# Optimization experiments

Measured on AMD Instinct MI355X. Metric: run time of the kernel, lower is better.

The kernel has to match this reference:

```python
import jax, jax.numpy as jnp
import numpy as np

B, N, D = 2, 2048, 1024
H, DH = 16, 64
DI = 4096
EPS = 1e-5
NEG_SLOPE = 0.01  # F.leaky_relu default


def _ln(x, g, b):
    mu = jnp.mean(x, axis=-1, keepdims=True)
    var = jnp.mean((x - mu) ** 2, axis=-1, keepdims=True)
    return (x - mu) * jax.lax.rsqrt(var + EPS) * g + b


def setup_inputs() -> dict:
    key = jax.random.key(0)
    ks = jax.random.split(key, 10)
    s = 0.02
    return {
        "Z": jax.random.normal(ks[0], (B, N, D), jnp.float32),
        "new_mask": jax.random.normal(ks[1], (B, N, N), jnp.float32),
        "mask": jax.random.uniform(ks[2], (B, N, N), jnp.float32),
        "ln1_g": jnp.ones((D,), jnp.float32),
        "ln1_b": jnp.zeros((D,), jnp.float32),
        "qkv_w": jax.random.normal(ks[3], (3 * D, D), jnp.float32) * s,
        "qkv_b": jnp.zeros((3 * D,), jnp.float32),
        "o_w": jax.random.normal(ks[4], (D, H * DH), jnp.float32) * s,
        "ln2_g": jnp.ones((D,), jnp.float32),
        "ln2_b": jnp.zeros((D,), jnp.float32),
        "p1_w": jax.random.normal(ks[5], (DI, D), jnp.float32) * s,
        "p1_b": jnp.zeros((DI,), jnp.float32),
        "p2_w": jax.random.normal(ks[6], (D, DI), jnp.float32) * s,
        "p2_b": jnp.zeros((D,), jnp.float32),
    }


def reference(Z, new_mask, mask, ln1_g, ln1_b, qkv_w, qkv_b, o_w, ln2_g, ln2_b, p1_w, p1_b, p2_w, p2_b):
    inp = Z
    Zn = _ln(Z, ln1_g, ln1_b)
    qkv = (Zn @ qkv_w.T + qkv_b).reshape(B, N, H, 3 * DH)
    # torch chunk order in the source: V, Q, K
    V, Q, K = jnp.split(qkv, 3, axis=3)  # each [B,N,H,DH]
    # scores: einsum('bnij,bmij->binm') == [B,H,N,N]
    W = jnp.einsum("bnhd,bmhd->bhnm", Q, K) / np.sqrt(DH) + new_mask[:, None]
    A = jax.nn.softmax(W, axis=3) * mask[:, None]
    attn = jnp.einsum("bhnm,bmhd->bnhd", A, V).reshape(B, N, D)
    attn = jnp.where(attn >= 0, attn, NEG_SLOPE * attn) @ o_w.T  # leaky_relu then o_net (no bias)
    Z1 = attn + inp
    Zn2 = _ln(Z1, ln2_g, ln2_b)
    h = jax.nn.relu(Zn2 @ p1_w.T + p1_b)
    return h @ p2_w.T + p2_b + Z1
```

## Files before the change

kernel.cpp:

```cpp
#include <hip/hip_runtime.h>

typedef unsigned short u16;
typedef __attribute__((ext_vector_type(8))) short bf16x8;
typedef __attribute__((ext_vector_type(4))) float f32x4;

#define DEV static __device__ __forceinline__

DEV u16 f2bf(float f) {
    unsigned u = __float_as_uint(f);
    u += 0x7FFFu + ((u >> 16) & 1u);
    return (u16)(u >> 16);
}

typedef const __attribute__((address_space(1))) void* gas1_t;
typedef __attribute__((address_space(3))) void* gas3_t;

DEV void gl_lds16(const u16* g, u16* l) {
    __builtin_amdgcn_global_load_lds((gas1_t)g, (gas3_t)l, 16, 0, 0);
}

DEV int sw8(int row, int chunk) { return row * 64 + ((chunk ^ (row & 7)) << 3); }

__global__ __launch_bounds__(256) void prep_all(const float* __restrict__ qkv_w,
                                                const float* __restrict__ o_w,
                                                const float* __restrict__ p1_w,
                                                const float* __restrict__ p2_w,
                                                const float* __restrict__ qkv_b,
                                                const float* __restrict__ nm,
                                                const float* __restrict__ pm,
                                                u16* __restrict__ qkvW,
                                                u16* __restrict__ oW,
                                                u16* __restrict__ p1W,
                                                u16* __restrict__ p2W,
                                                float* __restrict__ pbias,
                                                unsigned* __restrict__ Mp) {
    const int bid = blockIdx.x, t = threadIdx.x;
    if (bid < 3072) {
        int i = bid * 256 + t;
        int orow = i >> 8, cc = i & 255;
        int region = orow >> 10, rem = orow & 1023, h = rem >> 6, tt = rem & 63;
        int srow = h * 192 + region * 64 + tt;
        float4 v = ((const float4*)qkv_w)[srow * 256 + cc];
        ushort4 o;
        o.x = f2bf(v.x); o.y = f2bf(v.y); o.z = f2bf(v.z); o.w = f2bf(v.w);
        ((ushort4*)qkvW)[i] = o;
    } else if (bid < 4096) {
        int i = (bid - 3072) * 256 + t;
        float4 v = ((const float4*)o_w)[i];
        ushort4 o;
        o.x = f2bf(v.x); o.y = f2bf(v.y); o.z = f2bf(v.z); o.w = f2bf(v.w);
        ((ushort4*)oW)[i] = o;
    } else if (bid < 8192) {
        int i = (bid - 4096) * 256 + t;
        float4 v = ((const float4*)p1_w)[i];
        ushort4 o;
        o.x = f2bf(v.x); o.y = f2bf(v.y); o.z = f2bf(v.z); o.w = f2bf(v.w);
        ((ushort4*)p1W)[i] = o;
    } else if (bid < 12288) {
        int i = (bid - 8192) * 256 + t;
        float4 v = ((const float4*)p2_w)[i];
        ushort4 o;
        o.x = f2bf(v.x); o.y = f2bf(v.y); o.z = f2bf(v.z); o.w = f2bf(v.w);
        ((ushort4*)p2W)[i] = o;
    } else if (bid < 20480) {
        int i = (bid - 12288) * 256 + t;
        float4 a = ((const float4*)nm)[i];
        float4 b = ((const float4*)pm)[i];
        uint4 o;
        o.x = ((unsigned)f2bf(b.x) << 16) | f2bf(a.x * 1.4426950f);
        o.y = ((unsigned)f2bf(b.y) << 16) | f2bf(a.y * 1.4426950f);
        o.z = ((unsigned)f2bf(b.z) << 16) | f2bf(a.z * 1.4426950f);
        o.w = ((unsigned)f2bf(b.w) << 16) | f2bf(a.w * 1.4426950f);
        ((uint4*)Mp)[i] = o;
    } else {
#pragma unroll
        for (int k = 0; k < 12; k++) {
            int i = k * 256 + t;
            int region = i >> 10, rem = i & 1023, h = rem >> 6, tt = rem & 63;
            pbias[i] = qkv_b[h * 192 + region * 64 + tt];
        }
    }
}

__global__ __launch_bounds__(256) void ln_bf16(const float* __restrict__ x,
                                               const float* __restrict__ gam,
                                               const float* __restrict__ bet,
                                               u16* __restrict__ y) {
    const int row = blockIdx.x;
    const int t = threadIdx.x;
    const float4 v = ((const float4*)(x + (size_t)row * 1024))[t];
    float s = v.x + v.y + v.z + v.w;
    float ss = v.x * v.x + v.y * v.y + v.z * v.z + v.w * v.w;
#pragma unroll
    for (int o = 1; o < 64; o <<= 1) {
        s += __shfl_xor(s, o);
        ss += __shfl_xor(ss, o);
    }
    __shared__ float rs[4], rss[4];
    const int wave = t >> 6, lane = t & 63;
    if (lane == 0) { rs[wave] = s; rss[wave] = ss; }
    __syncthreads();
    const float tot = rs[0] + rs[1] + rs[2] + rs[3];
    const float totss = rss[0] + rss[1] + rss[2] + rss[3];
    const float mu = tot * (1.0f / 1024.0f);
    const float var = totss * (1.0f / 1024.0f) - mu * mu;
    const float rstd = rsqrtf(var + 1e-5f);
    const float4 g4 = ((const float4*)gam)[t];
    const float4 b4 = ((const float4*)bet)[t];
    ushort4 o;
    o.x = f2bf((v.x - mu) * rstd * g4.x + b4.x);
    o.y = f2bf((v.y - mu) * rstd * g4.y + b4.y);
    o.z = f2bf((v.z - mu) * rstd * g4.z + b4.z);
    o.w = f2bf((v.w - mu) * rstd * g4.w + b4.w);
    ((ushort4*)(y + (size_t)row * 1024))[t] = o;
}

__global__ __launch_bounds__(256) void ln2_comb4(const float* __restrict__ p0,
                                                 const float* __restrict__ p1,
                                                 const float* __restrict__ p2,
                                                 const float* __restrict__ p3,
                                                 const float* __restrict__ Z,
                                                 const float* __restrict__ gam,
                                                 const float* __restrict__ bet,
                                                 float* __restrict__ Z1,
                                                 u16* __restrict__ y) {
    const int row = blockIdx.x;
    const int t = threadIdx.x;
    const size_t off = (size_t)row * 256 + t;
    const float4 a = ((const float4*)p0)[off];
    const float4 c = ((const float4*)p1)[off];
    const float4 d = ((const float4*)p2)[off];
    const float4 e = ((const float4*)p3)[off];
    const float4 z = ((const float4*)Z)[off];
    float4 v;
    v.x = a.x + c.x + d.x + e.x + z.x;
    v.y = a.y + c.y + d.y + e.y + z.y;
    v.z = a.z + c.z + d.z + e.z + z.z;
    v.w = a.w + c.w + d.w + e.w + z.w;
    ((float4*)Z1)[off] = v;
    float s = v.x + v.y + v.z + v.w;
    float ss = v.x * v.x + v.y * v.y + v.z * v.z + v.w * v.w;
#pragma unroll
    for (int o = 1; o < 64; o <<= 1) {
        s += __shfl_xor(s, o);
        ss += __shfl_xor(ss, o);
    }
    __shared__ float rs[4], rss[4];
    const int wave = t >> 6, lane = t & 63;
    if (lane == 0) { rs[wave] = s; rss[wave] = ss; }
    __syncthreads();
    const float tot = rs[0] + rs[1] + rs[2] + rs[3];
    const float totss = rss[0] + rss[1] + rss[2] + rss[3];
    const float mu = tot * (1.0f / 1024.0f);
    const float var = totss * (1.0f / 1024.0f) - mu * mu;
    const float rstd = rsqrtf(var + 1e-5f);
    const float4 g4 = ((const float4*)gam)[t];
    const float4 b4 = ((const float4*)bet)[t];
    ushort4 o;
    o.x = f2bf((v.x - mu) * rstd * g4.x + b4.x);
    o.y = f2bf((v.y - mu) * rstd * g4.y + b4.y);
    o.z = f2bf((v.z - mu) * rstd * g4.z + b4.z);
    o.w = f2bf((v.w - mu) * rstd * g4.w + b4.w);
    ((ushort4*)(y + (size_t)row * 1024))[t] = o;
}

__global__ __launch_bounds__(256) void out_comb(const float* __restrict__ p0,
                                                const float* __restrict__ p1,
                                                const float* __restrict__ bias,
                                                const float* __restrict__ Z1,
                                                float* __restrict__ out) {
    int i = blockIdx.x * 256 + threadIdx.x;
    float4 a = ((const float4*)p0)[i];
    float4 c = ((const float4*)p1)[i];
    float4 z = ((const float4*)Z1)[i];
    float4 b = ((const float4*)bias)[i & 255];
    float4 o;
    o.x = a.x + c.x + z.x + b.x; o.y = a.y + c.y + z.y + b.y;
    o.z = a.z + c.z + z.z + b.z; o.w = a.w + c.w + z.w + b.w;
    ((float4*)out)[i] = o;
}

template <int EPI>
__global__ __launch_bounds__(256, 3) void gemm_bt(const u16* __restrict__ A,
                                                  const u16* __restrict__ Bt,
                                                  const float* __restrict__ bias,
                                                  void* __restrict__ out0,
                                                  void* __restrict__ out1,
                                                  void* __restrict__ out2,
                                                  int M, int N, int K, int ldk) {
    __shared__ __align__(16) u16 As[128 * 32];
    __shared__ __align__(16) u16 Bs[128 * 32];
    const int tid = threadIdx.x;
    const int wave = tid >> 6, lane = tid & 63;
    const int lhi = lane >> 4, llo = lane & 15;
    const int bx = blockIdx.x, by = blockIdx.y;
    const int kz = blockIdx.z * K;

    const int arow = wave * 32 + (lane >> 2);
    const int acol = (lane & 3) * 8;
    const u16* gA = A + (size_t)(by * 128 + arow) * ldk + kz + acol;
    const u16* gB = Bt + (size_t)(bx * 128 + arow) * ldk + kz + acol;
    u16* lA = As + wave * 1024 + lane * 8;
    u16* lB = Bs + wave * 1024 + lane * 8;

    const int wr = wave >> 1, wc = wave & 1;
    const f32x4 zero = {0.f, 0.f, 0.f, 0.f};
    f32x4 acc[4][4];
#pragma unroll
    for (int i = 0; i < 4; i++)
#pragma unroll
        for (int j = 0; j < 4; j++) acc[i][j] = zero;

    for (int k0 = 0; k0 < K; k0 += 32) {
        __syncthreads();
        gl_lds16(gA, lA);
        gl_lds16(gA + 16 * (size_t)ldk, lA + 512);
        gl_lds16(gB, lB);
        gl_lds16(gB + 16 * (size_t)ldk, lB + 512);
        gA += 32; gB += 32;
        __syncthreads();
        bf16x8 af[4], bfr[4];
#pragma unroll
        for (int i = 0; i < 4; i++)
            af[i] = *(const bf16x8*)(As + (wr * 64 + i * 16 + llo) * 32 + lhi * 8);
#pragma unroll
        for (int j = 0; j < 4; j++)
            bfr[j] = *(const bf16x8*)(Bs + (wc * 64 + j * 16 + llo) * 32 + lhi * 8);
#pragma unroll
        for (int i = 0; i < 4; i++)
#pragma unroll
            for (int j = 0; j < 4; j++)
                acc[i][j] = __builtin_amdgcn_mfma_f32_16x16x32_bf16(af[i], bfr[j], acc[i][j], 0, 0, 0);
    }

    const int rbase = by * 128 + wr * 64 + lhi * 4;
    const int cbase = bx * 128 + wc * 64 + llo;
    float* pout = nullptr;
    if constexpr (EPI == 4) {
        pout = (blockIdx.z < 2) ? ((float*)out0 + (size_t)blockIdx.z * M * N)
                                : ((float*)out1 + (size_t)(blockIdx.z - 2) * M * N);
    }
#pragma unroll
    for (int i = 0; i < 4; i++) {
#pragma unroll
        for (int j = 0; j < 4; j++) {
#pragma unroll
            for (int r = 0; r < 4; r++) {
                const int row = rbase + i * 16 + r;
                const int col = cbase + j * 16;
                float v = acc[i][j][r];
                if constexpr (EPI == 0) {
                    v += bias[col];
                    const int region = col >> 10;
                    const int c = col & 1023;
                    const int b = row >> 11, n = row & 2047;
                    if (region == 0) {
                        ((float*)out0)[(size_t)row * 1024 + c] = v;
                    } else {
                        const int h = c >> 6, t = c & 63;
                        u16* dst = (region == 1) ? (u16*)out1 : (u16*)out2;
                        dst[(((size_t)(b * 16 + h)) * 2048 + n) * 64 + t] = f2bf(v);
                    }
                } else if constexpr (EPI == 2) {
                    v += bias[col];
                    v = v > 0.f ? v : 0.f;
                    ((u16*)out0)[(size_t)row * N + col] = f2bf(v);
                } else {
                    pout[(size_t)row * N + col] = v;
                }
            }
        }
    }
}

__global__ __launch_bounds__(256) void vtrans(const float* __restrict__ Vsc,
                                              u16* __restrict__ Vt) {
    __shared__ u16 Ts[64 * 72];
    const int nt = blockIdx.x;
    const int bh = blockIdx.y;
    const int b = bh >> 4, h = bh & 15;
    const int t = threadIdx.x;
    const int n0 = nt * 64;
    const int nr = t >> 2;
    const int dq = (t & 3) * 16;
    const float* src = Vsc + ((size_t)(b * 2048 + n0 + nr)) * 1024 + h * 64 + dq;
    float4 v0 = ((const float4*)src)[0];
    float4 v1 = ((const float4*)src)[1];
    float4 v2 = ((const float4*)src)[2];
    float4 v3 = ((const float4*)src)[3];
    u16* c0 = Ts + nr;
    c0[(dq + 0) * 72]  = f2bf(v0.x); c0[(dq + 1) * 72]  = f2bf(v0.y);
    c0[(dq + 2) * 72]  = f2bf(v0.z); c0[(dq + 3) * 72]  = f2bf(v0.w);
    c0[(dq + 4) * 72]  = f2bf(v1.x); c0[(dq + 5) * 72]  = f2bf(v1.y);
    c0[(dq + 6) * 72]  = f2bf(v1.z); c0[(dq + 7) * 72]  = f2bf(v1.w);
    c0[(dq + 8) * 72]  = f2bf(v2.x); c0[(dq + 9) * 72]  = f2bf(v2.y);
    c0[(dq + 10) * 72] = f2bf(v2.z); c0[(dq + 11) * 72] = f2bf(v2.w);
    c0[(dq + 12) * 72] = f2bf(v3.x); c0[(dq + 13) * 72] = f2bf(v3.y);
    c0[(dq + 14) * 72] = f2bf(v3.z); c0[(dq + 15) * 72] = f2bf(v3.w);
    __syncthreads();
    const int d = t >> 2, n8 = (t & 3) * 16;
    bf16x8 o0 = *(const bf16x8*)(Ts + d * 72 + n8);
    bf16x8 o1 = *(const bf16x8*)(Ts + d * 72 + n8 + 8);
    u16* dst = Vt + ((size_t)bh * 64 + d) * 2048 + n0 + n8;
    *(bf16x8*)dst = o0;
    *(bf16x8*)(dst + 8) = o1;
}

__global__ __launch_bounds__(256, 4) void attn_fused4(const u16* __restrict__ Qg,
                                                      const u16* __restrict__ Kg,
                                                      const u16* __restrict__ Vt,
                                                      const unsigned* __restrict__ Mp,
                                                      u16* __restrict__ attnL) {
    __shared__ __align__(16) u16 Qs[64 * 64];
    __shared__ __align__(16) u16 Ks[64 * 64];
    __shared__ __align__(16) u16 Vs[64 * 64];
    __shared__ __align__(16) u16 Ps[64 * 72];
    const int tid = threadIdx.x, wave = tid >> 6, lane = tid & 63;
    const int lhi = lane >> 4, llo = lane & 15;
    const int id = blockIdx.x;
    const int hh = id >> 6, rem = id & 63;
    const int b = rem >> 5, qt = rem & 31;
    const int bh = b * 16 + hh;
    const int q0 = qt * 64;
    const int l3 = lane >> 3, l7 = lane & 7;
    const int swcol = (l7 ^ (l3 & 7)) * 8;

#pragma unroll
    for (int s = 0; s < 2; s++) {
        const int row = wave * 16 + s * 8 + l3;
        gl_lds16(Qg + ((size_t)bh * 2048 + q0 + row) * 64 + swcol,
                 Qs + wave * 1024 + s * 512 + lane * 8);
    }

    const unsigned* Mpb = Mp + (size_t)b * 2048 * 2048;
    int midx[4];
#pragma unroll
    for (int r = 0; r < 4; r++)
        midx[r] = (q0 + wave * 16 + lhi * 4 + r) * 2048 + llo;

    const f32x4 zero = {0.f, 0.f, 0.f, 0.f};
    f32x4 accO[4];
    float lsum[4];
#pragma unroll
    for (int j = 0; j < 4; j++) accO[j] = zero;
#pragma unroll
    for (int r = 0; r < 4; r++) lsum[r] = 0.f;

    const float CS = 0.125f * 1.4426950f;
    const int pb0 = (wave * 16 + lhi * 4) * 72 + llo;

    for (int m0 = 0; m0 < 2048; m0 += 64) {
        __syncthreads();
#pragma unroll
        for (int s = 0; s < 2; s++) {
            const int row = wave * 16 + s * 8 + l3;
            gl_lds16(Kg + ((size_t)bh * 2048 + m0 + row) * 64 + swcol,
                     Ks + wave * 1024 + s * 512 + lane * 8);
            gl_lds16(Vt + ((size_t)bh * 64 + row) * 2048 + m0 + swcol,
                     Vs + wave * 1024 + s * 512 + lane * 8);
        }
        unsigned mv[4][4];
#pragma unroll
        for (int r = 0; r < 4; r++)
#pragma unroll
            for (int j = 0; j < 4; j++) mv[r][j] = Mpb[midx[r] + m0 + j * 16];
        __syncthreads();

        f32x4 sacc[4];
#pragma unroll
        for (int j = 0; j < 4; j++) sacc[j] = zero;
#pragma unroll
        for (int kk = 0; kk < 2; kk++) {
            const bf16x8 aq = *(const bf16x8*)(Qs + sw8(wave * 16 + llo, kk * 4 + lhi));
#pragma unroll
            for (int j = 0; j < 4; j++) {
                const bf16x8 bk = *(const bf16x8*)(Ks + sw8(j * 16 + llo, kk * 4 + lhi));
                sacc[j] = __builtin_amdgcn_mfma_f32_16x16x32_bf16(aq, bk, sacc[j], 0, 0, 0);
            }
        }

#pragma unroll
        for (int j = 0; j < 4; j++)
#pragma unroll
            for (int r = 0; r < 4; r++) {
                const unsigned u = mv[r][j];
                const float nm = __uint_as_float(u << 16);
                const float pm = __uint_as_float(u & 0xFFFF0000u);
                const float e = exp2f(fmaf(sacc[j][r], CS, nm));
                lsum[r] += e;
                const float p = e * pm;
                Ps[pb0 + r * 72 + j * 16] = (u16)(__float_as_uint(p) >> 16);
            }

#pragma unroll
        for (int kk = 0; kk < 2; kk++) {
            const bf16x8 ap = *(const bf16x8*)(Ps + (wave * 16 + llo) * 72 + kk * 32 + lhi * 8);
#pragma unroll
            for (int jd = 0; jd < 4; jd++) {
                const bf16x8 bv = *(const bf16x8*)(Vs + sw8(jd * 16 + llo, kk * 4 + lhi));
                accO[jd] = __builtin_amdgcn_mfma_f32_16x16x32_bf16(ap, bv, accO[jd], 0, 0, 0);
            }
        }
    }

#pragma unroll
    for (int r = 0; r < 4; r++) {
#pragma unroll
        for (int o = 1; o < 16; o <<= 1) lsum[r] += __shfl_xor(lsum[r], o);
        lsum[r] = 1.0f / lsum[r];
    }
#pragma unroll
    for (int jd = 0; jd < 4; jd++)
#pragma unroll
        for (int r = 0; r < 4; r++) {
            float v = accO[jd][r] * lsum[r];
            v = v >= 0.f ? v : 0.01f * v;
            const int q = q0 + wave * 16 + lhi * 4 + r;
            attnL[((size_t)b * 2048 + q) * 1024 + hh * 64 + jd * 16 + llo] = f2bf(v);
        }
}

extern "C" void kernel_launch(void* const* d_in, const int* in_sizes, int n_in,
                              void* d_out, int out_size, void* d_ws, size_t ws_size,
                              hipStream_t stream) {
    const float* Z     = (const float*)d_in[0];
    const float* nmask = (const float*)d_in[1];
    const float* pmask = (const float*)d_in[2];
    const float* ln1_g = (const float*)d_in[3];
    const float* ln1_b = (const float*)d_in[4];
    const float* qkv_w = (const float*)d_in[5];
    const float* qkv_b = (const float*)d_in[6];
    const float* o_w   = (const float*)d_in[7];
    const float* ln2_g = (const float*)d_in[8];
    const float* ln2_b = (const float*)d_in[9];
    const float* p1_w  = (const float*)d_in[10];
    const float* p1_b  = (const float*)d_in[11];
    const float* p2_w  = (const float*)d_in[12];
    const float* p2_b  = (const float*)d_in[13];
    float* out = (float*)d_out;

    char* w = (char*)d_ws;
    auto take = [&](size_t bytes) -> char* {
        char* p = w;
        w += (bytes + 255) & ~(size_t)255;
        return p;
    };
    u16* qkvW   = (u16*)take((size_t)3072 * 1024 * 2);
    u16* oW     = (u16*)take((size_t)1024 * 1024 * 2);
    u16* p1W    = (u16*)take((size_t)4096 * 1024 * 2);
    u16* p2W    = (u16*)take((size_t)1024 * 4096 * 2);
    u16* Zn     = (u16*)take((size_t)4096 * 1024 * 2);
    u16* Qb     = (u16*)take((size_t)32 * 2048 * 64 * 2);
    u16* Kb     = (u16*)take((size_t)32 * 2048 * 64 * 2);
    u16* Vt     = (u16*)take((size_t)32 * 64 * 2048 * 2);
    u16* attnL  = (u16*)take((size_t)4096 * 1024 * 2);
    float* Z1   = (float*)take((size_t)4096 * 1024 * 4);
    u16* hbuf   = (u16*)take((size_t)4096 * 4096 * 2);
    unsigned* Mp = (unsigned*)take((size_t)2 * 2048 * 2048 * 4);
    float* pbias = (float*)take((size_t)3072 * 4);
    float* Vsc    = (float*)hbuf;
    float* part01 = (float*)Mp;
    float* part23 = (float*)hbuf;

    prep_all<<<dim3(20481), 256, 0, stream>>>(qkv_w, o_w, p1_w, p2_w, qkv_b, nmask, pmask,
                                              qkvW, oW, p1W, p2W, pbias, Mp);
    ln_bf16<<<dim3(4096), 256, 0, stream>>>(Z, ln1_g, ln1_b, Zn);
    gemm_bt<0><<<dim3(24, 32), 256, 0, stream>>>(Zn, qkvW, pbias, Vsc, Qb, Kb, 4096, 3072, 1024, 1024);
    vtrans<<<dim3(32, 32), 256, 0, stream>>>(Vsc, Vt);
    attn_fused4<<<dim3(1024), 256, 0, stream>>>(Qb, Kb, Vt, Mp, attnL);
    gemm_bt<4><<<dim3(8, 32, 4), 256, 0, stream>>>(attnL, oW, nullptr, part01, part23, nullptr,
                                                   4096, 1024, 256, 1024);
    ln2_comb4<<<dim3(4096), 256, 0, stream>>>(part01, part01 + (size_t)4096 * 1024,
                                              part23, part23 + (size_t)4096 * 1024,
                                              Z, ln2_g, ln2_b, Z1, Zn);
    gemm_bt<2><<<dim3(32, 32), 256, 0, stream>>>(Zn, p1W, p1_b, hbuf, nullptr, nullptr,
                                                 4096, 4096, 1024, 1024);
    gemm_bt<4><<<dim3(8, 32, 2), 256, 0, stream>>>(hbuf, p2W, nullptr, part01, nullptr, nullptr,
                                                   4096, 1024, 2048, 4096);
    out_comb<<<dim3(4096), 256, 0, stream>>>(part01, part01 + (size_t)4096 * 1024, p2_b, Z1, out);
}
```

Before: 442.2 us.

## Rewrite attention with 32x32 MFMA, register P, double-buffered K/V, tiled mask layout

Result: slower. 458.8 us (+3.7%).

```diff
diff --git a/kernel.cpp b/kernel.cpp
--- a/kernel.cpp
+++ b/kernel.cpp
@@ -3,6 +3,8 @@
 typedef unsigned short u16;
 typedef __attribute__((ext_vector_type(8))) short bf16x8;
 typedef __attribute__((ext_vector_type(4))) float f32x4;
+typedef __attribute__((ext_vector_type(16))) float f32x16;
+typedef __attribute__((ext_vector_type(4))) unsigned u32x4;
 
 #define DEV static __device__ __forceinline__
 
@@ -17,6 +19,12 @@
 
 DEV void gl_lds16(const u16* g, u16* l) {
     __builtin_amdgcn_global_load_lds((gas1_t)g, (gas3_t)l, 16, 0, 0);
+}
+
+DEV unsigned cvtpk_bf16(float a, float b) {
+    unsigned r;
+    asm("v_cvt_pk_bf16_f32 %0, %1, %2" : "=v"(r) : "v"(a), "v"(b));
+    return r;
 }
 
 DEV int sw8(int row, int chunk) { return row * 64 + ((chunk ^ (row & 7)) << 3); }
@@ -71,7 +79,17 @@
         o.y = ((unsigned)f2bf(b.y) << 16) | f2bf(a.y * 1.4426950f);
         o.z = ((unsigned)f2bf(b.z) << 16) | f2bf(a.z * 1.4426950f);
         o.w = ((unsigned)f2bf(b.w) << 16) | f2bf(a.w * 1.4426950f);
-        ((uint4*)Mp)[i] = o;
+        int e = i * 4;
+        int bb = e >> 22;
+        int rem = e & 4194303;
+        int n = rem >> 11;
+        int m = rem & 2047;
+        int mt = m >> 5;
+        int j = m & 31;
+        int hi = (j >> 2) & 1;
+        int rb4 = j >> 3;
+        size_t oi = (((size_t)(bb * 64 + mt) * 2048 + n) * 2 + hi) * 4 + rb4;
+        ((uint4*)Mp)[oi] = o;
     } else {
 #pragma unroll
         for (int k = 0; k < 12; k++) {
@@ -306,118 +324,151 @@
     *(bf16x8*)(dst + 8) = o1;
 }
 
-__global__ __launch_bounds__(256, 4) void attn_fused4(const u16* __restrict__ Qg,
+DEV void stage_kv(const u16* __restrict__ Kg, const u16* __restrict__ Vtg,
+                  u16* ks, u16* vs, int bh, int m0, int wave, int lane) {
+    const int l3 = lane >> 3, l7 = lane & 7;
+    const int swcol = (l7 ^ l3) << 3;
+#pragma unroll
+    for (int s = 0; s < 2; s++) {
+        const int row = wave * 16 + s * 8 + l3;
+        gl_lds16(Kg + ((size_t)bh * 2048 + m0 + row) * 64 + swcol,
+                 ks + wave * 1024 + s * 512 + lane * 8);
+        gl_lds16(Vtg + ((size_t)bh * 64 + row) * 2048 + m0 + swcol,
+                 vs + wave * 1024 + s * 512 + lane * 8);
+    }
+}
+
+__global__ __launch_bounds__(256, 4) void attn_fused5(const u16* __restrict__ Qg,
                                                       const u16* __restrict__ Kg,
-                                                      const u16* __restrict__ Vt,
+                                                      const u16* __restrict__ Vtg,
                                                       const unsigned* __restrict__ Mp,
                                                       u16* __restrict__ attnL) {
-    __shared__ __align__(16) u16 Qs[64 * 64];
-    __shared__ __align__(16) u16 Ks[64 * 64];
-    __shared__ __align__(16) u16 Vs[64 * 64];
-    __shared__ __align__(16) u16 Ps[64 * 72];
+    __shared__ __align__(16) u16 Ks[2][64 * 64];
+    __shared__ __align__(16) u16 Vs[2][64 * 64];
+    __shared__ float lsh[2][32], lsh2[2][32];
     const int tid = threadIdx.x, wave = tid >> 6, lane = tid & 63;
-    const int lhi = lane >> 4, llo = lane & 15;
+    const int qh = wave & 1, wm = wave >> 1;
+    const int hi = lane >> 5, l31 = lane & 31;
     const int id = blockIdx.x;
     const int hh = id >> 6, rem = id & 63;
     const int b = rem >> 5, qt = rem & 31;
     const int bh = b * 16 + hh;
     const int q0 = qt * 64;
-    const int l3 = lane >> 3, l7 = lane & 7;
-    const int swcol = (l7 ^ (l3 & 7)) * 8;
-
-#pragma unroll
-    for (int s = 0; s < 2; s++) {
-        const int row = wave * 16 + s * 8 + l3;
-        gl_lds16(Qg + ((size_t)bh * 2048 + q0 + row) * 64 + swcol,
-                 Qs + wave * 1024 + s * 512 + lane * 8);
-    }
-
-    const unsigned* Mpb = Mp + (size_t)b * 2048 * 2048;
-    int midx[4];
-#pragma unroll
-    for (int r = 0; r < 4; r++)
-        midx[r] = (q0 + wave * 16 + lhi * 4 + r) * 2048 + llo;
-
-    const f32x4 zero = {0.f, 0.f, 0.f, 0.f};
-    f32x4 accO[4];
-    float lsum[4];
-#pragma unroll
-    for (int j = 0; j < 4; j++) accO[j] = zero;
-#pragma unroll
-    for (int r = 0; r < 4; r++) lsum[r] = 0.f;
-
+
+    stage_kv(Kg, Vtg, Ks[0], Vs[0], bh, 0, wave, lane);
+    const int qrow = q0 + qh * 32 + l31;
+    const u16* qptr = Qg + ((size_t)bh * 2048 + qrow) * 64 + hi * 8;
+    bf16x8 qf[4];
+#pragma unroll
+    for (int ks = 0; ks < 4; ks++) qf[ks] = *(const bf16x8*)(qptr + ks * 16);
+
+    const unsigned* mptr = Mp + (size_t)b * 4194304 + (size_t)wm * 65536
+                              + (size_t)qrow * 32 + hi * 16;
+
+    const f32x16 z16 = {0.f,0.f,0.f,0.f,0.f,0.f,0.f,0.f,0.f,0.f,0.f,0.f,0.f,0.f,0.f,0.f};
+    f32x16 accO[2];
+    accO[0] = z16; accO[1] = z16;
+    float lsum = 0.f;
     const float CS = 0.125f * 1.4426950f;
-    const int pb0 = (wave * 16 + lhi * 4) * 72 + llo;
-
-    for (int m0 = 0; m0 < 2048; m0 += 64) {
+    const bool h1 = (hi != 0);
+    __syncthreads();
+
+    for (int t = 0; t < 32; t++) {
+        const int cur = t & 1;
+        const uint4* mp4 = (const uint4*)(mptr + (size_t)t * 131072);
+        const uint4 mva = mp4[0], mvb = mp4[1], mvc = mp4[2], mvd = mp4[3];
+        if (t < 31) stage_kv(Kg, Vtg, Ks[cur ^ 1], Vs[cur ^ 1], bh, (t + 1) * 64, wave, lane);
+
+        const u16* ksb = Ks[cur];
+        f32x16 sacc = z16;
+        __builtin_amdgcn_s_setprio(1);
+#pragma unroll
+        for (int ks = 0; ks < 4; ks++) {
+            const bf16x8 kf = *(const bf16x8*)(ksb + sw8(wm * 32 + l31, ks * 2 + hi));
+            sacc = __builtin_amdgcn_mfma_f32_32x32x16_bf16(kf, qf[ks], sacc, 0, 0, 0);
+        }
+        __builtin_amdgcn_s_setprio(0);
+
+        const unsigned mm[16] = {mva.x, mva.y, mva.z, mva.w, mvb.x, mvb.y, mvb.z, mvb.w,
+                                 mvc.x, mvc.y, mvc.z, mvc.w, mvd.x, mvd.y, mvd.z, mvd.w};
+        float p[16];
+#pragma unroll
+        for (int r = 0; r < 16; r++) {
+            const unsigned u = mm[r];
+            const float e = exp2f(fmaf(sacc[r], CS, __uint_as_float(u << 16)));
+            lsum += e;
+            p[r] = e * __uint_as_float(u & 0xFFFF0000u);
+        }
+        const unsigned w0 = cvtpk_bf16(p[0], p[1]),   w1 = cvtpk_bf16(p[2], p[3]);
+        const unsigned w2 = cvtpk_bf16(p[4], p[5]),   w3 = cvtpk_bf16(p[6], p[7]);
+        const unsigned w4 = cvtpk_bf16(p[8], p[9]),   w5 = cvtpk_bf16(p[10], p[11]);
+        const unsigned w6 = cvtpk_bf16(p[12], p[13]), w7 = cvtpk_bf16(p[14], p[15]);
+        const unsigned o0 = (unsigned)__shfl_xor((int)w0, 32);
+        const unsigned o1 = (unsigned)__shfl_xor((int)w1, 32);
+        const unsigned o2 = (unsigned)__shfl_xor((int)w2, 32);
+        const unsigned o3 = (unsigned)__shfl_xor((int)w3, 32);
+        const unsigned o4 = (unsigned)__shfl_xor((int)w4, 32);
+        const unsigned o5 = (unsigned)__shfl_xor((int)w5, 32);
+        const unsigned o6 = (unsigned)__shfl_xor((int)w6, 32);
+        const unsigned o7 = (unsigned)__shfl_xor((int)w7, 32);
+        const u32x4 fa0 = {h1 ? o2 : w0, h1 ? o3 : w1, h1 ? w2 : o0, h1 ? w3 : o1};
+        const u32x4 fa1 = {h1 ? o6 : w4, h1 ? o7 : w5, h1 ? w6 : o4, h1 ? w7 : o5};
+        const bf16x8 pa0 = __builtin_bit_cast(bf16x8, fa0);
+        const bf16x8 pa1 = __builtin_bit_cast(bf16x8, fa1);
+
+        const u16* vsb = Vs[cur];
+        __builtin_amdgcn_s_setprio(1);
+#pragma unroll
+        for (int dh = 0; dh < 2; dh++) {
+            const bf16x8 vf0 = *(const bf16x8*)(vsb + sw8(dh * 32 + l31, wm * 4 + hi));
+            accO[dh] = __builtin_amdgcn_mfma_f32_32x32x16_bf16(pa0, vf0, accO[dh], 0, 0, 0);
+            const bf16x8 vf1 = *(const bf16x8*)(vsb + sw8(dh * 32 + l31, wm * 4 + 2 + hi));
+            accO[dh] = __builtin_amdgcn_mfma_f32_32x32x16_bf16(pa1, vf1, accO[dh], 0, 0, 0);
+        }
+        __builtin_amdgcn_s_setprio(0);
         __syncthreads();
-#pragma unroll
-        for (int s = 0; s < 2; s++) {
-            const int row = wave * 16 + s * 8 + l3;
-            gl_lds16(Kg + ((size_t)bh * 2048 + m0 + row) * 64 + swcol,
-                     Ks + wave * 1024 + s * 512 + lane * 8);
-            gl_lds16(Vt + ((size_t)bh * 64 + row) * 2048 + m0 + swcol,
-                     Vs + wave * 1024 + s * 512 + lane * 8);
-        }
-        unsigned mv[4][4];
-#pragma unroll
-        for (int r = 0; r < 4; r++)
-#pragma unroll
-            for (int j = 0; j < 4; j++) mv[r][j] = Mpb[midx[r] + m0 + j * 16];
-        __syncthreads();
-
-        f32x4 sacc[4];
-#pragma unroll
-        for (int j = 0; j < 4; j++) sacc[j] = zero;
-#pragma unroll
-        for (int kk = 0; kk < 2; kk++) {
-            const bf16x8 aq = *(const bf16x8*)(Qs + sw8(wave * 16 + llo, kk * 4 + lhi));
-#pragma unroll
-            for (int j = 0; j < 4; j++) {
-                const bf16x8 bk = *(const bf16x8*)(Ks + sw8(j * 16 + llo, kk * 4 + lhi));
-                sacc[j] = __builtin_amdgcn_mfma_f32_16x16x32_bf16(aq, bk, sacc[j], 0, 0, 0);
+    }
+
+    const float lsum2 = lsum + __shfl_xor(lsum, 32);
+    float* cb = (float*)&Ks[0][0];
+    if (wm == 1) {
+        float* dst = cb + (size_t)(qh * 64 + lane) * 32;
+#pragma unroll
+        for (int dh = 0; dh < 2; dh++)
+#pragma unroll
+            for (int c = 0; c < 4; c++) {
+                const f32x4 v = {accO[dh][c * 4 + 0], accO[dh][c * 4 + 1],
+                                 accO[dh][c * 4 + 2], accO[dh][c * 4 + 3]};
+                *(f32x4*)(dst + dh * 16 + c * 4) = v;
+            }
+        if (lane < 32) lsh[qh][lane] = lsum2;
+    }
+    __syncthreads();
+    if (wm == 0) {
+        const float* src = cb + (size_t)(qh * 64 + lane) * 32;
+        const float lt = lsum2 + lsh[qh][l31];
+#pragma unroll
+        for (int dh = 0; dh < 2; dh++)
+#pragma unroll
+            for (int c = 0; c < 16; c++)
+                accO[dh][c] += src[dh * 16 + c];
+        if (lane < 32) lsh2[qh][lane] = 1.0f / lt;
+    }
+    __syncthreads();
+    if (wm == 0) {
+#pragma unroll
+        for (int r = 0; r < 16; r++) {
+            const int ql = (r & 3) + 8 * (r >> 2) + 4 * hi;
+            const float linv = lsh2[qh][ql];
+            const int qg = q0 + qh * 32 + ql;
+#pragma unroll
+            for (int dh = 0; dh < 2; dh++) {
+                float v = accO[dh][r] * linv;
+                v = v >= 0.f ? v : 0.01f * v;
+                attnL[((size_t)b * 2048 + qg) * 1024 + hh * 64 + dh * 32 + l31] = f2bf(v);
             }
         }
-
-#pragma unroll
-        for (int j = 0; j < 4; j++)
-#pragma unroll
-            for (int r = 0; r < 4; r++) {
-                const unsigned u = mv[r][j];
-                const float nm = __uint_as_float(u << 16);
-                const float pm = __uint_as_float(u & 0xFFFF0000u);
-                const float e = exp2f(fmaf(sacc[j][r], CS, nm));
-                lsum[r] += e;
-                const float p = e * pm;
-                Ps[pb0 + r * 72 + j * 16] = (u16)(__float_as_uint(p) >> 16);
-            }
-
-#pragma unroll
-        for (int kk = 0; kk < 2; kk++) {
-            const bf16x8 ap = *(const bf16x8*)(Ps + (wave * 16 + llo) * 72 + kk * 32 + lhi * 8);
-#pragma unroll
-            for (int jd = 0; jd < 4; jd++) {
-                const bf16x8 bv = *(const bf16x8*)(Vs + sw8(jd * 16 + llo, kk * 4 + lhi));
-                accO[jd] = __builtin_amdgcn_mfma_f32_16x16x32_bf16(ap, bv, accO[jd], 0, 0, 0);
-            }
-        }
-    }
-
-#pragma unroll
-    for (int r = 0; r < 4; r++) {
-#pragma unroll
-        for (int o = 1; o < 16; o <<= 1) lsum[r] += __shfl_xor(lsum[r], o);
-        lsum[r] = 1.0f / lsum[r];
-    }
-#pragma unroll
-    for (int jd = 0; jd < 4; jd++)
-#pragma unroll
-        for (int r = 0; r < 4; r++) {
-            float v = accO[jd][r] * lsum[r];
-            v = v >= 0.f ? v : 0.01f * v;
-            const int q = q0 + wave * 16 + lhi * 4 + r;
-            attnL[((size_t)b * 2048 + q) * 1024 + hh * 64 + jd * 16 + llo] = f2bf(v);
-        }
+    }
 }
 
 extern "C" void kernel_launch(void* const* d_in, const int* in_sizes, int n_in,
@@ -467,7 +518,7 @@
     ln_bf16<<<dim3(4096), 256, 0, stream>>>(Z, ln1_g, ln1_b, Zn);
     gemm_bt<0><<<dim3(24, 32), 256, 0, stream>>>(Zn, qkvW, pbias, Vsc, Qb, Kb, 4096, 3072, 1024, 1024);
     vtrans<<<dim3(32, 32), 256, 0, stream>>>(Vsc, Vt);
-    attn_fused4<<<dim3(1024), 256, 0, stream>>>(Qb, Kb, Vt, Mp, attnL);
+    attn_fused5<<<dim3(1024), 256, 0, stream>>>(Qb, Kb, Vt, Mp, attnL);
     gemm_bt<4><<<dim3(8, 32, 4), 256, 0, stream>>>(attnL, oW, nullptr, part01, part23, nullptr,
                                                    4096, 1024, 256, 1024);
     ln2_comb4<<<dim3(4096), 256, 0, stream>>>(part01, part01 + (size_t)4096 * 1024,
```
